# Kernel tuning notes

Measured on AMD Instinct MI355X. Metric: run time of the kernel, lower is better.

The kernel has to match this reference:

```python
import jax, jax.numpy as jnp
import numpy as np
from jax import lax

B, N, C_IN = 8, 16384, 32
NPOINT = 1024
RADII = (0.5, 1.0)
NSAMPLES = (16, 32)
MLPS = ((35, 32, 64), (35, 64, 128))  # first dim includes +3 for use_xyz


def setup_inputs():
    key = jax.random.key(0)
    ks = jax.random.split(key, 20)
    inp = {
        'xyz': jax.random.normal(ks[0], (B, N, 3), jnp.float32),
        'features': jax.random.normal(ks[1], (B, C_IN, N), jnp.float32),
    }
    i = 2
    for bi, spec in enumerate(MLPS):
        for li in range(len(spec) - 1):
            cin, cout = spec[li], spec[li + 1]
            inp['w%d_%d' % (bi, li)] = jax.random.normal(ks[i], (cout, cin), jnp.float32) * np.float32(1.0 / np.sqrt(cin)); i += 1
            inp['s%d_%d' % (bi, li)] = jax.random.uniform(ks[i], (cout,), jnp.float32, minval=0.5, maxval=1.5); i += 1
            inp['b%d_%d' % (bi, li)] = jax.random.normal(ks[i], (cout,), jnp.float32) * 0.1; i += 1
    return inp


def _fps(xyz, npoint):
    # iterative D-FPS, start from index 0 (matches CUDA furthest_point_sampling)
    Bb, Nn, _ = xyz.shape
    def body(carry, _):
        dists, far = carry
        centroid = jnp.take_along_axis(xyz, far[:, None, None], axis=1)  # (B,1,3)
        d = jnp.sum((xyz - centroid) ** 2, axis=-1)                       # (B,N)
        dists = jnp.minimum(dists, d)
        return (dists, jnp.argmax(dists, axis=-1).astype(jnp.int32)), far
    init = (jnp.full((Bb, Nn), 1e10, jnp.float32), jnp.zeros((Bb,), jnp.int32))
    _, idx = lax.scan(body, init, None, length=npoint)
    return idx.T  # (B, npoint)


def _ball_query(dist2, radius, nsample):
    # first-nsample-in-index-order semantics of pointnet2 ball_query;
    # empty slots padded with first hit (0 if no hit at all)
    Nn = dist2.shape[-1]
    scores = jnp.where(dist2 < radius * radius, jnp.arange(Nn, dtype=jnp.int32), Nn)
    neg, _ = lax.top_k(-scores, nsample)  # nsample smallest indices
    idx = -neg
    first = jnp.where(idx[..., :1] == Nn, 0, idx[..., :1])
    return jnp.where(idx == Nn, first, idx)


def _forward(xyz, features, params):
    fwx = jnp.concatenate([xyz.transpose(0, 2, 1), features], axis=1)   # (B,3+C,N)
    fps_idx = _fps(xyz, NPOINT)                                          # (B,P) int32
    new_xyz = jnp.take_along_axis(xyz, fps_idx[:, :, None], axis=1)      # (B,P,3)
    # pairwise squared distances via gemm (B,P,N)
    xx = jnp.sum(xyz * xyz, axis=-1)
    qq = jnp.sum(new_xyz * new_xyz, axis=-1)
    dist2 = qq[:, :, None] + xx[:, None, :] - 2.0 * jnp.einsum('bpd,bnd->bpn', new_xyz, xyz)
    centers = new_xyz.transpose(0, 2, 1)[..., None]                      # (B,3,P,1)
    outs = []
    for k in range(len(RADII)):
        idx = _ball_query(dist2, RADII[k], NSAMPLES[k])                  # (B,P,S)
        grouped = jax.vmap(lambda f, i: f[:, i])(fwx, idx)               # (B,3+C,P,S)
        x = jnp.concatenate([grouped[:, :3] - centers, grouped[:, 3:]], axis=1)
        for (w, s, b) in params[k]:
            # 1x1 Conv2d (no bias) + eval-mode BN folded into (s,b) + ReLU
            x = jax.nn.relu(jnp.einsum('oc,bcps->bops', w, x) * s[None, :, None, None] + b[None, :, None, None])
        outs.append(jnp.max(x, axis=-1))                                 # max_pool over nsample
    return new_xyz, jnp.concatenate(outs, axis=1)                        # (B,P,3), (B,192,P)


def reference(xyz, features, w0_0, s0_0, b0_0, w0_1, s0_1, b0_1, w1_0, s1_0, b1_0, w1_1, s1_1, b1_1):
    params = [[(w0_0, s0_0, b0_0), (w0_1, s0_1, b0_1)],
              [(w1_0, s1_0, b1_0), (w1_1, s1_1, b1_1)]]
    return _forward(xyz, features, params)
```

## Files before the change

### kernel.cpp

```cpp
#include <hip/hip_runtime.h>

#define B 8
#define N 16384
#define C_IN 32
#define P 1024

typedef float v2f __attribute__((ext_vector_type(2)));
typedef unsigned long long ull;

#define R8(OP) OP(0) OP(1) OP(2) OP(3) OP(4) OP(5) OP(6) OP(7)

__device__ __forceinline__ v2f pk_add(v2f a, v2f b) {
  v2f d; asm("v_pk_add_f32 %0, %1, %2" : "=v"(d) : "v"(a), "v"(b)); return d;
}
__device__ __forceinline__ v2f pk_mul(v2f a, v2f b) {
  v2f d; asm("v_pk_mul_f32 %0, %1, %2" : "=v"(d) : "v"(a), "v"(b)); return d;
}
__device__ __forceinline__ float negf(float x) {
  return __int_as_float(__float_as_int(x) ^ 0x80000000);
}

template <int CTRL>
__device__ __forceinline__ float dpp_fmax(float v) {
  float o = __int_as_float(__builtin_amdgcn_update_dpp(
      __float_as_int(v), __float_as_int(v), CTRL, 0xF, 0xF, false));
  return fmaxf(v, o);
}

__global__ __launch_bounds__(1024)
void fps_kernel(const float* __restrict__ xyz, float* __restrict__ new_xyz)
{
  __shared__ __align__(16) float sx[N];
  __shared__ __align__(16) float sy[N];
  __shared__ ull slot[2];

  const int b = blockIdx.x;
  const int t = threadIdx.x;
  const float* xb = xyz + (size_t)b * (N * 3);

  if (t == 0) { slot[0] = ~0ull; slot[1] = ~0ull; }

#define FPS_DECL(j) v2f pzp##j, dmp##j; dmp##j.x = 1e10f; dmp##j.y = 1e10f;
  R8(FPS_DECL)
#define FPS_LOADP(j) {                                                         \
    const int n0 = (t << 2) + ((j >> 1) << 12) + ((j & 1) << 1);               \
    const float2 ld0 = *(const float2*)&xb[(size_t)n0 * 3 + 0];     \
    const float2 ld1 = *(const float2*)&xb[(size_t)n0 * 3 + 2];     \
    const float2 ld2 = *(const float2*)&xb[(size_t)n0 * 3 + 4];     \
    sx[n0]     = ld0.x;  sy[n0]     = ld0.y;                                   \
    sx[n0 + 1] = ld1.y;  sy[n0 + 1] = ld2.x;                                   \
    pzp##j.x   = ld1.x;  pzp##j.y   = ld2.y;                                   \
    asm volatile("" : "+v"(pzp##j)); }
  R8(FPS_LOADP)

  float cz = xb[2];
  __syncthreads();
  float cx = sx[0], cy = sy[0];
  int sel = 0, msel = 0;

  for (int iter = 0; iter < P; ++iter) {
    msel = (t == iter) ? sel : msel;
    if (iter == P - 1) break;

    v2f cxx, cyy, czz;
    { float v = negf(cx); cxx.x = v; cxx.y = v; }
    { float v = negf(cy); cyy.x = v; cyy.y = v; }
    { float v = negf(cz); czz.x = v; czz.y = v; }

    v2f sq0, sq1, sq2, sq3, sq4, sq5, sq6, sq7;
#define FPS_XY(i, ja, jb) {                                                    \
      const int n0 = (t << 2) + ((i) << 12);                                   \
      v2f xl = *(const v2f*)&sx[n0];  v2f xh = *(const v2f*)&sx[n0 + 2];       \
      v2f yl = *(const v2f*)&sy[n0];  v2f yh = *(const v2f*)&sy[n0 + 2];       \
      v2f dxl = pk_add(xl, cxx), dyl = pk_add(yl, cyy);                        \
      v2f dxh = pk_add(xh, cxx), dyh = pk_add(yh, cyy);                        \
      sq##ja = pk_add(pk_mul(dxl, dxl), pk_mul(dyl, dyl));                     \
      sq##jb = pk_add(pk_mul(dxh, dxh), pk_mul(dyh, dyh)); }
    FPS_XY(0, 0, 1)
    FPS_XY(1, 2, 3)
    FPS_XY(2, 4, 5)
    FPS_XY(3, 6, 7)

    float bestv = -1.0f;
    int   s = 0;
#define FPS_Z(j) {                                                             \
      v2f dz = pk_add(pzp##j, czz);                                            \
      v2f dd = pk_add(sq##j, pk_mul(dz, dz));                                  \
      dmp##j.x = fminf(dmp##j.x, dd.x);                                        \
      dmp##j.y = fminf(dmp##j.y, dd.y);                                        \
      bool b0 = dmp##j.x > bestv;                                              \
      bestv = b0 ? dmp##j.x : bestv;  s = b0 ? (2 * (j))     : s;              \
      bool b1 = dmp##j.y > bestv;                                              \
      bestv = b1 ? dmp##j.y : bestv;  s = b1 ? (2 * (j) + 1) : s; }
    R8(FPS_Z)

    float wm = bestv;
    wm = dpp_fmax<0xB1>(wm);
    wm = dpp_fmax<0x4E>(wm);
    wm = dpp_fmax<0x141>(wm);
    wm = dpp_fmax<0x140>(wm);
    wm = dpp_fmax<0x142>(wm);
    wm = dpp_fmax<0x143>(wm);
    const float wmax = __int_as_float(
        __builtin_amdgcn_readlane(__float_as_int(wm), 63));

    if (bestv == wmax) {
      int nn = (t << 2) + ((s & 12) << 10) + (s & 3);
      unsigned inv = ~__float_as_uint(bestv);
      ull key = ((ull)(unsigned)(P - 1 - iter) << 46) |
                ((ull)inv << 14) | (ull)(unsigned)nn;
      atomicMin(&slot[iter & 1], key);
    }
    __syncthreads();

    ull k = slot[iter & 1];
    sel = __builtin_amdgcn_readfirstlane((int)((unsigned)k & 0x3FFFu));
    cx = sx[sel];
    cy = sy[sel];
    cz = xb[(size_t)sel * 3 + 2];
  }

  {
    const int n = msel;
    size_t o = ((size_t)b * P + t) * 3;
    new_xyz[o + 0] = sx[n];
    new_xyz[o + 1] = sy[n];
    new_xyz[o + 2] = xb[(size_t)n * 3 + 2];
  }
#undef FPS_DECL
#undef FPS_LOADP
#undef FPS_XY
#undef FPS_Z
}

__global__ __launch_bounds__(256) void tr_kernel(
    const float* __restrict__ feats, float* __restrict__ ftr)
{
  __shared__ float tile[32][65];
  const int tid = threadIdx.x;
  const int b  = blockIdx.x >> 8;
  const int n0 = (blockIdx.x & 255) << 6;
  const float* fb = feats + (size_t)b * (C_IN * N);

  const int c  = tid >> 3;
  const int nn = (tid & 7) << 3;
  const float* src = fb + (size_t)c * N + n0 + nn;
  const float4 a0 = *(const float4*)(src);
  const float4 a1 = *(const float4*)(src + 4);
  tile[c][nn + 0] = a0.x; tile[c][nn + 1] = a0.y;
  tile[c][nn + 2] = a0.z; tile[c][nn + 3] = a0.w;
  tile[c][nn + 4] = a1.x; tile[c][nn + 5] = a1.y;
  tile[c][nn + 6] = a1.z; tile[c][nn + 7] = a1.w;
  __syncthreads();

  const int n  = tid >> 2;
  const int c0 = (tid & 3) << 3;
  float4 o0, o1;
  o0.x = tile[c0 + 0][n]; o0.y = tile[c0 + 1][n];
  o0.z = tile[c0 + 2][n]; o0.w = tile[c0 + 3][n];
  o1.x = tile[c0 + 4][n]; o1.y = tile[c0 + 5][n];
  o1.z = tile[c0 + 6][n]; o1.w = tile[c0 + 7][n];
  float4* dst = (float4*)(ftr + ((size_t)b * N + n0 + n) * 32 + c0);
  dst[0] = o0;
  dst[1] = o1;
}

__global__ __launch_bounds__(256) void ballq_kernel(
    const float* __restrict__ xyz, const float* __restrict__ new_xyz,
    int* __restrict__ idx0, int* __restrict__ idx1)
{
  const int wid  = blockIdx.x * 4 + (threadIdx.x >> 6);
  const int lane = threadIdx.x & 63;
  const int b = wid >> 10;
  const int p = wid & (P - 1);
  const float* xb = xyz + (size_t)b * (N * 3);
  const size_t bp = (size_t)b * P + p;
  const float cx = new_xyz[bp * 3 + 0];
  const float cy = new_xyz[bp * 3 + 1];
  const float cz = new_xyz[bp * 3 + 2];
  const float qv = __fadd_rn(__fadd_rn(__fmul_rn(cx, cx), __fmul_rn(cy, cy)),
                             __fmul_rn(cz, cz));
  int* __restrict__ o0 = idx0 + bp * 16;
  int* __restrict__ o1 = idx1 + bp * 32;

  int c0 = 0, c1 = 0, f0 = 0, f1 = 0;
  const unsigned long long below = (1ull << lane) - 1ull;

  for (int base = 0; base < N; base += 64) {
    int n = base + lane;
    float x = xb[n * 3 + 0], y = xb[n * 3 + 1], z = xb[n * 3 + 2];
    float xxv = __fadd_rn(__fadd_rn(__fmul_rn(x, x), __fmul_rn(y, y)),
                          __fmul_rn(z, z));
    float dot = __fadd_rn(__fadd_rn(__fmul_rn(cx, x), __fmul_rn(cy, y)),
                          __fmul_rn(cz, z));
    float d2 = __fsub_rn(__fadd_rn(qv, xxv), __fmul_rn(2.0f, dot));
    unsigned long long m0 = __ballot(d2 < 0.25f);
    unsigned long long m1 = __ballot(d2 < 1.0f);
    if (c0 == 0 && m0) f0 = base + __builtin_ctzll(m0);
    if (c1 == 0 && m1) f1 = base + __builtin_ctzll(m1);
    if ((m0 >> lane) & 1ull) {
      int pos = c0 + (int)__builtin_popcountll(m0 & below);
      if (pos < 16) o0[pos] = n;
    }
    if ((m1 >> lane) & 1ull) {
      int pos = c1 + (int)__builtin_popcountll(m1 & below);
      if (pos < 32) o1[pos] = n;
    }
    c0 = min(16, c0 + (int)__builtin_popcountll(m0));
    c1 = min(32, c1 + (int)__builtin_popcountll(m1));
    if (c0 >= 16 && c1 >= 32) break;
  }
  for (int s = c0 + lane; s < 16; s += 64) o0[s] = f0;
  for (int s = c1 + lane; s < 32; s += 64) o1[s] = f1;
}

template <int S, int C1, int C2, int CH_OFF>
__global__ __launch_bounds__(256) void mlp_kernel(
    const float* __restrict__ xyz, const float* __restrict__ ftr,
    const float* __restrict__ new_xyz, const int* __restrict__ idx,
    const float* __restrict__ w1, const float* __restrict__ s1,
    const float* __restrict__ b1, const float* __restrict__ w2,
    const float* __restrict__ s2, const float* __restrict__ b2,
    float* __restrict__ out)
{
  static_assert((C1 * S) % 512 == 0 && (C2 * S) % 512 == 0, "mapping");
  __shared__ float wl1[35][C1];
  __shared__ float wl2[C1][C2 + 1];
  __shared__ float sb1[2][C1];
  __shared__ float sb2[2][C2];
  __shared__ float xs[35][S];
  __shared__ float o1s[C1][S];
  __shared__ float pm[256];

  const int tid = threadIdx.x;
  for (int i = tid; i < 35 * C1; i += 256) {
    int o = i % C1, c = i / C1;
    wl1[c][o] = w1[o * 35 + c];
  }
  for (int i = tid; i < (C1 * C2) / 4; i += 256) {
    const float4 v = *(const float4*)&w2[i * 4];
    const int o = (i * 4) / C1, c = (i * 4) % C1;
    wl2[c + 0][o] = v.x; wl2[c + 1][o] = v.y;
    wl2[c + 2][o] = v.z; wl2[c + 3][o] = v.w;
  }
  if (tid < C1) { sb1[0][tid] = s1[tid]; sb1[1][tid] = b1[tid]; }
  if (tid < C2) { sb2[0][tid] = s2[tid]; sb2[1][tid] = b2[tid]; }

  const int b  = blockIdx.x / (P / 8);
  const int p0 = (blockIdx.x % (P / 8)) * 8;
  const float* xb = xyz + (size_t)b * (N * 3);
  const float* fb = ftr + (size_t)b * N * 32;
  __syncthreads();

  for (int pi = 0; pi < 8; ++pi) {
    const int p = p0 + pi;
    const size_t bp = (size_t)b * P + p;
    const int* ip = idx + bp * S;
    const float cx = new_xyz[bp * 3 + 0];
    const float cy = new_xyz[bp * 3 + 1];
    const float cz = new_xyz[bp * 3 + 2];
    for (int s2 = tid; s2 < S; s2 += 256) {
      const int n = ip[s2];
      xs[0][s2] = xb[n * 3 + 0] - cx;
      xs[1][s2] = xb[n * 3 + 1] - cy;
      xs[2][s2] = xb[n * 3 + 2] - cz;
    }
    for (int i = tid; i < S * 8; i += 256) {
      const int s = i >> 3, q = i & 7;
      const int n = ip[s];
      const float4 v = *(const float4*)&fb[(size_t)n * 32 + q * 4];
      const int c = 3 + q * 4;
      xs[c + 0][s] = v.x; xs[c + 1][s] = v.y;
      xs[c + 2][s] = v.z; xs[c + 3][s] = v.w;
    }
    __syncthreads();
    {
      constexpr int OPT  = (C1 * S) / 256;
      constexpr int OPT2 = OPT / 2;
      const int s  = tid % S;
      const int ob = (tid / S) * OPT;
      v2f acc[OPT2];
#pragma unroll
      for (int m = 0; m < OPT2; ++m) { acc[m].x = 0.0f; acc[m].y = 0.0f; }
      for (int c = 0; c < 35; ++c) {
        const float xv = xs[c][s];
        v2f xv2; xv2.x = xv; xv2.y = xv;
#pragma unroll
        for (int m = 0; m < OPT2; ++m) {
          const v2f w = *(const v2f*)&wl1[c][ob + 2 * m];
          asm("v_pk_fma_f32 %0, %1, %2, %0"
              : "+v"(acc[m]) : "v"(xv2), "v"(w));
        }
      }
#pragma unroll
      for (int m = 0; m < OPT2; ++m) {
        const int o0i = ob + 2 * m, o1i = ob + 2 * m + 1;
        float v0 = fmaf(acc[m].x, sb1[0][o0i], sb1[1][o0i]);
        float v1 = fmaf(acc[m].y, sb1[0][o1i], sb1[1][o1i]);
        o1s[o0i][s] = fmaxf(v0, 0.0f);
        o1s[o1i][s] = fmaxf(v1, 0.0f);
      }
    }
    __syncthreads();
    {
      constexpr int NS  = (C2 * S) / 256;
      constexpr int NS2 = NS / 2;
      const int o2 = tid % C2;
      const int sb = (tid / C2) * NS;
      v2f acc[NS2];
#pragma unroll
      for (int m = 0; m < NS2; ++m) { acc[m].x = 0.0f; acc[m].y = 0.0f; }
      for (int c = 0; c < C1; ++c) {
        const float wv = wl2[c][o2];
        v2f wv2; wv2.x = wv; wv2.y = wv;
#pragma unroll
        for (int m = 0; m < NS2; ++m) {
          const v2f ov = *(const v2f*)&o1s[c][sb + 2 * m];
          asm("v_pk_fma_f32 %0, %1, %2, %0"
              : "+v"(acc[m]) : "v"(wv2), "v"(ov));
        }
      }
      const float scale = sb2[0][o2], bias = sb2[1][o2];
      float m2 = 0.0f;
#pragma unroll
      for (int m = 0; m < NS2; ++m) {
        m2 = fmaxf(m2, fmaf(acc[m].x, scale, bias));
        m2 = fmaxf(m2, fmaf(acc[m].y, scale, bias));
      }
      pm[tid] = m2;
      __syncthreads();
      if (tid < C2) {
        float mm = pm[tid];
#pragma unroll
        for (int g = 1; g < 256 / C2; ++g) mm = fmaxf(mm, pm[tid + g * C2]);
        out[((size_t)b * 192 + CH_OFF + tid) * P + p] = mm;
      }
    }
    __syncthreads();
  }
}

extern "C" void kernel_launch(void* const* d_in, const int* in_sizes, int n_in,
                              void* d_out, int out_size, void* d_ws, size_t ws_size,
                              hipStream_t stream) {
  const float* xyz   = (const float*)d_in[0];
  const float* feats = (const float*)d_in[1];
  const float* w0_0 = (const float*)d_in[2];
  const float* s0_0 = (const float*)d_in[3];
  const float* b0_0 = (const float*)d_in[4];
  const float* w0_1 = (const float*)d_in[5];
  const float* s0_1 = (const float*)d_in[6];
  const float* b0_1 = (const float*)d_in[7];
  const float* w1_0 = (const float*)d_in[8];
  const float* s1_0 = (const float*)d_in[9];
  const float* b1_0 = (const float*)d_in[10];
  const float* w1_1 = (const float*)d_in[11];
  const float* s1_1 = (const float*)d_in[12];
  const float* b1_1 = (const float*)d_in[13];

  float* out      = (float*)d_out;
  float* new_xyz  = out;
  float* feat_out = out + (size_t)B * P * 3;

  char* w = (char*)d_ws;
  float* ftr = (float*)w; w += (size_t)B * N * 32 * sizeof(float);
  int* idx0 = (int*)w; w += (size_t)B * P * 16 * sizeof(int);
  int* idx1 = (int*)w; w += (size_t)B * P * 32 * sizeof(int);

  tr_kernel<<<dim3(B * (N / 64)), dim3(256), 0, stream>>>(feats, ftr);
  fps_kernel<<<dim3(B), dim3(1024), 0, stream>>>(xyz, new_xyz);
  ballq_kernel<<<dim3(B * P / 4), dim3(256), 0, stream>>>(xyz, new_xyz, idx0, idx1);
  mlp_kernel<16, 32, 64, 0><<<dim3(B * P / 8), dim3(256), 0, stream>>>(
      xyz, ftr, new_xyz, idx0, w0_0, s0_0, b0_0, w0_1, s0_1, b0_1, feat_out);
  mlp_kernel<32, 64, 128, 64><<<dim3(B * P / 8), dim3(256), 0, stream>>>(
      xyz, ftr, new_xyz, idx1, w1_0, s1_0, b1_0, w1_1, s1_1, b1_1, feat_out);
}
```

Before: 2.308 ms.

## Fuse feature transpose into FPS launch and vectorize ball query over SoA xyz

Merges the feature-transpose kernel into the FPS launch as extra blocks, so the transpose runs on idle CUs while the 8 long-running FPS blocks execute. Those extra blocks also write a structure-of-arrays copy of xyz. The ball query reads that SoA copy with float4 loads and handles 4 points per lane per iteration, cutting loop trips and ballot overhead. The costs are extra workspace and extra write traffic for the SoA copy. The transpose blocks now run at 1024 threads each with 256-column tiles.

```diff
diff --git a/kernel.cpp b/kernel.cpp
--- a/kernel.cpp
+++ b/kernel.cpp
@@ -28,14 +28,63 @@
 }
 
 __global__ __launch_bounds__(1024)
-void fps_kernel(const float* __restrict__ xyz, float* __restrict__ new_xyz)
+void fps_prep_kernel(const float* __restrict__ xyz,
+                     const float* __restrict__ feats,
+                     float* __restrict__ new_xyz,
+                     float* __restrict__ ftr,
+                     float* __restrict__ sox, float* __restrict__ soy,
+                     float* __restrict__ soz)
 {
-  __shared__ __align__(16) float sx[N];
-  __shared__ __align__(16) float sy[N];
-  __shared__ ull slot[2];
+  __shared__ __align__(16) char smem[131088];
+  const int t = threadIdx.x;
+
+  if (blockIdx.x >= 8) {
+    const int pid   = blockIdx.x - 8;
+    const int pb    = pid >> 6;
+    const int n0    = (pid & 63) << 8;
+    const float* fb = feats + (size_t)pb * (C_IN * N);
+    const float* xb = xyz + (size_t)pb * (N * 3);
+    float (*tile)[257] = (float(*)[257])smem;
+
+    {
+      const int c  = t >> 5;
+      const int nn = (t & 31) << 3;
+      const float* src = fb + (size_t)c * N + n0 + nn;
+      const float4 a0 = *(const float4*)(src);
+      const float4 a1 = *(const float4*)(src + 4);
+      tile[c][nn + 0] = a0.x; tile[c][nn + 1] = a0.y;
+      tile[c][nn + 2] = a0.z; tile[c][nn + 3] = a0.w;
+      tile[c][nn + 4] = a1.x; tile[c][nn + 5] = a1.y;
+      tile[c][nn + 6] = a1.z; tile[c][nn + 7] = a1.w;
+    }
+    if (t < 256) {
+      const int n = n0 + t;
+      const size_t o = (size_t)pb * N + n;
+      sox[o] = xb[(size_t)n * 3 + 0];
+      soy[o] = xb[(size_t)n * 3 + 1];
+      soz[o] = xb[(size_t)n * 3 + 2];
+    }
+    __syncthreads();
+    {
+      const int n  = t >> 2;
+      const int c0 = (t & 3) << 3;
+      float4 o0, o1;
+      o0.x = tile[c0 + 0][n]; o0.y = tile[c0 + 1][n];
+      o0.z = tile[c0 + 2][n]; o0.w = tile[c0 + 3][n];
+      o1.x = tile[c0 + 4][n]; o1.y = tile[c0 + 5][n];
+      o1.z = tile[c0 + 6][n]; o1.w = tile[c0 + 7][n];
+      float4* dst = (float4*)(ftr + ((size_t)pb * N + n0 + n) * 32 + c0);
+      dst[0] = o0;
+      dst[1] = o1;
+    }
+    return;
+  }
+
+  float* sx = (float*)smem;
+  float* sy = sx + N;
+  ull*  slot = (ull*)(smem + 2 * N * sizeof(float));
 
   const int b = blockIdx.x;
-  const int t = threadIdx.x;
   const float* xb = xyz + (size_t)b * (N * 3);
 
   if (t == 0) { slot[0] = ~0ull; slot[1] = ~0ull; }
@@ -133,47 +182,18 @@
 #undef FPS_Z
 }
 
-__global__ __launch_bounds__(256) void tr_kernel(
-    const float* __restrict__ feats, float* __restrict__ ftr)
-{
-  __shared__ float tile[32][65];
-  const int tid = threadIdx.x;
-  const int b  = blockIdx.x >> 8;
-  const int n0 = (blockIdx.x & 255) << 6;
-  const float* fb = feats + (size_t)b * (C_IN * N);
-
-  const int c  = tid >> 3;
-  const int nn = (tid & 7) << 3;
-  const float* src = fb + (size_t)c * N + n0 + nn;
-  const float4 a0 = *(const float4*)(src);
-  const float4 a1 = *(const float4*)(src + 4);
-  tile[c][nn + 0] = a0.x; tile[c][nn + 1] = a0.y;
-  tile[c][nn + 2] = a0.z; tile[c][nn + 3] = a0.w;
-  tile[c][nn + 4] = a1.x; tile[c][nn + 5] = a1.y;
-  tile[c][nn + 6] = a1.z; tile[c][nn + 7] = a1.w;
-  __syncthreads();
-
-  const int n  = tid >> 2;
-  const int c0 = (tid & 3) << 3;
-  float4 o0, o1;
-  o0.x = tile[c0 + 0][n]; o0.y = tile[c0 + 1][n];
-  o0.z = tile[c0 + 2][n]; o0.w = tile[c0 + 3][n];
-  o1.x = tile[c0 + 4][n]; o1.y = tile[c0 + 5][n];
-  o1.z = tile[c0 + 6][n]; o1.w = tile[c0 + 7][n];
-  float4* dst = (float4*)(ftr + ((size_t)b * N + n0 + n) * 32 + c0);
-  dst[0] = o0;
-  dst[1] = o1;
-}
-
 __global__ __launch_bounds__(256) void ballq_kernel(
-    const float* __restrict__ xyz, const float* __restrict__ new_xyz,
+    const float* __restrict__ sox, const float* __restrict__ soy,
+    const float* __restrict__ soz, const float* __restrict__ new_xyz,
     int* __restrict__ idx0, int* __restrict__ idx1)
 {
   const int wid  = blockIdx.x * 4 + (threadIdx.x >> 6);
   const int lane = threadIdx.x & 63;
   const int b = wid >> 10;
   const int p = wid & (P - 1);
-  const float* xb = xyz + (size_t)b * (N * 3);
+  const float* X = sox + (size_t)b * N;
+  const float* Y = soy + (size_t)b * N;
+  const float* Z = soz + (size_t)b * N;
   const size_t bp = (size_t)b * P + p;
   const float cx = new_xyz[bp * 3 + 0];
   const float cy = new_xyz[bp * 3 + 1];
@@ -184,30 +204,69 @@
   int* __restrict__ o1 = idx1 + bp * 32;
 
   int c0 = 0, c1 = 0, f0 = 0, f1 = 0;
-  const unsigned long long below = (1ull << lane) - 1ull;
-
-  for (int base = 0; base < N; base += 64) {
-    int n = base + lane;
-    float x = xb[n * 3 + 0], y = xb[n * 3 + 1], z = xb[n * 3 + 2];
-    float xxv = __fadd_rn(__fadd_rn(__fmul_rn(x, x), __fmul_rn(y, y)),
-                          __fmul_rn(z, z));
-    float dot = __fadd_rn(__fadd_rn(__fmul_rn(cx, x), __fmul_rn(cy, y)),
-                          __fmul_rn(cz, z));
-    float d2 = __fsub_rn(__fadd_rn(qv, xxv), __fmul_rn(2.0f, dot));
-    unsigned long long m0 = __ballot(d2 < 0.25f);
-    unsigned long long m1 = __ballot(d2 < 1.0f);
-    if (c0 == 0 && m0) f0 = base + __builtin_ctzll(m0);
-    if (c1 == 0 && m1) f1 = base + __builtin_ctzll(m1);
-    if ((m0 >> lane) & 1ull) {
-      int pos = c0 + (int)__builtin_popcountll(m0 & below);
-      if (pos < 16) o0[pos] = n;
-    }
-    if ((m1 >> lane) & 1ull) {
-      int pos = c1 + (int)__builtin_popcountll(m1 & below);
-      if (pos < 32) o1[pos] = n;
-    }
-    c0 = min(16, c0 + (int)__builtin_popcountll(m0));
-    c1 = min(32, c1 + (int)__builtin_popcountll(m1));
+  const ull below = (1ull << lane) - 1ull;
+
+  for (int base = 0; base < N; base += 256) {
+    const int n0 = base + (lane << 2);
+    const float4 xv = *(const float4*)&X[n0];
+    const float4 yv = *(const float4*)&Y[n0];
+    const float4 zv = *(const float4*)&Z[n0];
+
+    float d2[4];
+#pragma unroll
+    for (int e = 0; e < 4; ++e) {
+      const float x = (e == 0) ? xv.x : (e == 1) ? xv.y : (e == 2) ? xv.z : xv.w;
+      const float y = (e == 0) ? yv.x : (e == 1) ? yv.y : (e == 2) ? yv.z : yv.w;
+      const float z = (e == 0) ? zv.x : (e == 1) ? zv.y : (e == 2) ? zv.z : zv.w;
+      const float xx = __fadd_rn(__fadd_rn(__fmul_rn(x, x), __fmul_rn(y, y)),
+                                 __fmul_rn(z, z));
+      const float dot = __fadd_rn(__fadd_rn(__fmul_rn(cx, x), __fmul_rn(cy, y)),
+                                  __fmul_rn(cz, z));
+      d2[e] = __fsub_rn(__fadd_rn(qv, xx), __fmul_rn(2.0f, dot));
+    }
+
+    ull m0[4], m1[4];
+#pragma unroll
+    for (int e = 0; e < 4; ++e) {
+      m0[e] = __ballot(d2[e] < 0.25f);
+      m1[e] = __ballot(d2[e] < 1.0f);
+    }
+
+#define BQ_PROC(m, cap, oarr, cnt, fst) {                                      \
+    const int tot = (int)(__builtin_popcountll(m[0]) +                         \
+                          __builtin_popcountll(m[1]) +                         \
+                          __builtin_popcountll(m[2]) +                         \
+                          __builtin_popcountll(m[3]));                         \
+    if (cnt < cap && tot) {                                                    \
+      if (cnt == 0) {                                                          \
+        const ull any = m[0] | m[1] | m[2] | m[3];                             \
+        const int lm = __builtin_ctzll(any);                                   \
+        const int em = ((m[0] >> lm) & 1ull) ? 0 :                             \
+                       ((m[1] >> lm) & 1ull) ? 1 :                             \
+                       ((m[2] >> lm) & 1ull) ? 2 : 3;                          \
+        fst = base + (lm << 2) + em;                                           \
+      }                                                                        \
+      int pos = cnt + (int)(__builtin_popcountll(m[0] & below) +               \
+                            __builtin_popcountll(m[1] & below) +               \
+                            __builtin_popcountll(m[2] & below) +               \
+                            __builtin_popcountll(m[3] & below));               \
+      const bool h0 = (m[0] >> lane) & 1ull;                                   \
+      const bool h1 = (m[1] >> lane) & 1ull;                                   \
+      const bool h2 = (m[2] >> lane) & 1ull;                                   \
+      const bool h3 = (m[3] >> lane) & 1ull;                                   \
+      if (h0 && pos < cap) oarr[pos] = n0 + 0;                                 \
+      pos += h0;                                                               \
+      if (h1 && pos < cap) oarr[pos] = n0 + 1;                                 \
+      pos += h1;                                                               \
+      if (h2 && pos < cap) oarr[pos] = n0 + 2;                                 \
+      pos += h2;                                                               \
+      if (h3 && pos < cap) oarr[pos] = n0 + 3;                                 \
+    }                                                                          \
+    cnt = min(cap, cnt + tot); }
+
+    BQ_PROC(m0, 16, o0, c0, f0)
+    BQ_PROC(m1, 32, o1, c1, f1)
+#undef BQ_PROC
     if (c0 >= 16 && c1 >= 32) break;
   }
   for (int s = c0 + lane; s < 16; s += 64) o0[s] = f0;
@@ -259,11 +318,11 @@
     const float cx = new_xyz[bp * 3 + 0];
     const float cy = new_xyz[bp * 3 + 1];
     const float cz = new_xyz[bp * 3 + 2];
-    for (int s2 = tid; s2 < S; s2 += 256) {
-      const int n = ip[s2];
-      xs[0][s2] = xb[n * 3 + 0] - cx;
-      xs[1][s2] = xb[n * 3 + 1] - cy;
-      xs[2][s2] = xb[n * 3 + 2] - cz;
+    for (int s2i = tid; s2i < S; s2i += 256) {
+      const int n = ip[s2i];
+      xs[0][s2i] = xb[n * 3 + 0] - cx;
+      xs[1][s2i] = xb[n * 3 + 1] - cy;
+      xs[2][s2i] = xb[n * 3 + 2] - cz;
     }
     for (int i = tid; i < S * 8; i += 256) {
       const int s = i >> 3, q = i & 7;
@@ -364,12 +423,16 @@
 
   char* w = (char*)d_ws;
   float* ftr = (float*)w; w += (size_t)B * N * 32 * sizeof(float);
+  float* sox = (float*)w; w += (size_t)B * N * sizeof(float);
+  float* soy = (float*)w; w += (size_t)B * N * sizeof(float);
+  float* soz = (float*)w; w += (size_t)B * N * sizeof(float);
   int* idx0 = (int*)w; w += (size_t)B * P * 16 * sizeof(int);
   int* idx1 = (int*)w; w += (size_t)B * P * 32 * sizeof(int);
 
-  tr_kernel<<<dim3(B * (N / 64)), dim3(256), 0, stream>>>(feats, ftr);
-  fps_kernel<<<dim3(B), dim3(1024), 0, stream>>>(xyz, new_xyz);
-  ballq_kernel<<<dim3(B * P / 4), dim3(256), 0, stream>>>(xyz, new_xyz, idx0, idx1);
+  fps_prep_kernel<<<dim3(8 + B * (N / 256)), dim3(1024), 0, stream>>>(
+      xyz, feats, new_xyz, ftr, sox, soy, soz);
+  ballq_kernel<<<dim3(B * P / 4), dim3(256), 0, stream>>>(
+      sox, soy, soz, new_xyz, idx0, idx1);
   mlp_kernel<16, 32, 64, 0><<<dim3(B * P / 8), dim3(256), 0, stream>>>(
       xyz, ftr, new_xyz, idx0, w0_0, s0_0, b0_0, w0_1, s0_1, b0_1, feat_out);
   mlp_kernel<32, 64, 128, 64><<<dim3(B * P / 8), dim3(256), 0, stream>>>(
```

Result: faster. 2.193 ms (-5.0%).
